# Kernel optimization log

Measured on AMD Instinct MI355X. Metric: run time of the kernel, lower is better.

The kernel has to match this reference:

```python
import jax, jax.numpy as jnp
import numpy as np

N_NODES = 100000
D = 128


def gcn_conv(x, W, b, src, dst, deg_inv_sqrt):
    # PyG GCNConv: linear transform, symmetric-normalized aggregation with self-loops, bias
    h = x @ W  # [N, D_out]
    norm = deg_inv_sqrt[src] * deg_inv_sqrt[dst]  # [E_tot]
    msgs = h[src] * norm[:, None]  # gather + scale  [E_tot, D_out]
    out = jax.ops.segment_sum(msgs, dst, num_segments=x.shape[0])  # scatter-add to targets
    return out + b


def _prep_edges(edge_index, n_nodes):
    # add self-loops (weight 1) and compute deg^{-1/2} over targets (flow source_to_target)
    loops = jnp.arange(n_nodes, dtype=edge_index.dtype)
    src = jnp.concatenate([edge_index[0], loops])
    dst = jnp.concatenate([edge_index[1], loops])
    deg = jax.ops.segment_sum(jnp.ones_like(dst, dtype=jnp.float32), dst, num_segments=n_nodes)
    deg_inv_sqrt = jnp.where(deg > 0, jax.lax.rsqrt(jnp.maximum(deg, 1.0)), 0.0)
    return src, dst, deg_inv_sqrt


def setup_inputs() -> dict:
    key = jax.random.key(0)
    ks = jax.random.split(key, 8)
    node_fts = jax.random.normal(ks[0], (N_NODES, D), dtype=jnp.float32)
    edge_index = jax.random.randint(ks[1], (2, 1600000), 0, N_NODES, dtype=jnp.int64)
    scale = 1.0 / np.sqrt(D)
    W1 = jax.random.uniform(ks[2], (D, D), jnp.float32, -scale, scale)
    b1 = jnp.zeros((D,), jnp.float32)
    W2 = jax.random.uniform(ks[3], (D, D), jnp.float32, -scale, scale)
    b2 = jnp.zeros((D,), jnp.float32)
    W3 = jax.random.uniform(ks[4], (D, D), jnp.float32, -scale, scale)
    b3 = jnp.zeros((D,), jnp.float32)
    return {"node_fts": node_fts, "edge_index": edge_index,
            "W1": W1, "b1": b1, "W2": W2, "b2": b2, "W3": W3, "b3": b3}


def reference(node_fts, edge_index, W1, b1, W2, b2, W3, b3):
    n = node_fts.shape[0]
    src, dst, dinv = _prep_edges(edge_index, n)
    x = jax.nn.relu(gcn_conv(node_fts, W1, b1, src, dst, dinv))
    x = jax.nn.relu(gcn_conv(x, W2, b2, src, dst, dinv))
    x = jax.nn.relu(gcn_conv(x, W3, b3, src, dst, dinv))
    return x
```

## Files before the change

kernel.cpp:

```cpp
#include <hip/hip_runtime.h>

#define NN 100000
#define EE 1600000
#define NPART 8
#define PSZ (NN / NPART)
#define NI4 (EE / 4)
#define SUBW 196
#define NSB (NPART * 64)
#define SCAP 4096
#define RCAP 8192
#define LBCAP 96
#define ROWCAP 64
#define WTB 48

typedef __attribute__((ext_vector_type(8))) short bf16x8;
typedef __attribute__((ext_vector_type(4))) float f32x4;

__device__ inline unsigned int f2bf2(float a, float b) {
    unsigned int ua = __float_as_uint(a);
    unsigned int ub = __float_as_uint(b);
    ua = (ua + 0x7fffu + ((ua >> 16) & 1u)) >> 16;
    ub = (ub + 0x7fffu + ((ub >> 16) & 1u)) >> 16;
    return ua | (ub << 16);
}
__device__ inline unsigned short f2bf(float a) {
    unsigned int u = __float_as_uint(a);
    return (unsigned short)((u + 0x7fffu + ((u >> 16) & 1u)) >> 16);
}
__device__ inline float2 bf2f2(unsigned int u) {
    return make_float2(__uint_as_float(u << 16), __uint_as_float(u & 0xffff0000u));
}


__global__ __launch_bounds__(256) void fbwt_kernel(const int4* __restrict__ src4,
                                                   const int4* __restrict__ dst4,
                                                   int* __restrict__ gcur2,
                                                   uint2* __restrict__ buckets2,
                                                   const float* __restrict__ W1,
                                                   const float* __restrict__ W2,
                                                   const float* __restrict__ W3,
                                                   unsigned short* __restrict__ wt1,
                                                   unsigned short* __restrict__ wt2,
                                                   unsigned short* __restrict__ wt3,
                                                   unsigned int* __restrict__ hb,
                                                   float* __restrict__ dinv) {
    __shared__ uint2 bins[64][LBCAP];
    __shared__ int bcnt[64];
    __shared__ int gbase[64];
    __shared__ float tile[32][33];
    const int bx = blockIdx.x;

    if (bx < WTB) {
        const int m = bx >> 4;
        const int tl = bx & 15;
        const int ti = tl >> 2, tj = tl & 3;
        const float* W = m == 0 ? W1 : (m == 1 ? W2 : W3);
        unsigned short* wt = m == 0 ? wt1 : (m == 1 ? wt2 : wt3);
        const int r = threadIdx.x >> 5, c = threadIdx.x & 31;
#pragma unroll
        for (int rr = r; rr < 32; rr += 8)
            tile[rr][c] = W[(ti * 32 + rr) * 128 + tj * 32 + c];
        __syncthreads();
#pragma unroll
        for (int rr = r; rr < 32; rr += 8)
            wt[(size_t)(tj * 32 + rr) * 128 + ti * 32 + c] = f2bf(tile[c][rr]);
        if (bx == 0) {
            if (threadIdx.x < 64) hb[(size_t)NN * 64 + threadIdx.x] = 0;
            if (threadIdx.x == 64) dinv[NN] = 0.0f;
        }
        return;
    }

    const int fb = bx - WTB;
    const int p = fb >> 6;
    const int c = fb & 63;
    if (threadIdx.x < 64) bcnt[threadIdx.x] = 0;
    __syncthreads();
    const int lo = p * PSZ, hi = lo + PSZ;
    const int chunk4 = NI4 / 64;
    const int a0 = c * chunk4, a1 = a0 + chunk4;
    for (int i = a0 + threadIdx.x; i < a1; i += 256) {
        int4 d4 = dst4[i];
        bool m0 = (d4.x >= lo && d4.x < hi);
        bool m1 = (d4.y >= lo && d4.y < hi);
        bool m2 = (d4.z >= lo && d4.z < hi);
        bool m3 = (d4.w >= lo && d4.w < hi);
        if (!(m0 | m1 | m2 | m3)) continue;
        int4 s4 = src4[i];
        int ss[4] = {s4.x, s4.y, s4.z, s4.w};
        int dd[4] = {d4.x, d4.y, d4.z, d4.w};
        bool mm[4] = {m0, m1, m2, m3};
#pragma unroll
        for (int k = 0; k < 4; ++k) {
            if (!mm[k]) continue;
            int li = (dd[k] - lo) / SUBW;
            int pos = atomicAdd(&bcnt[li], 1);
            if (pos < LBCAP) {
                bins[li][pos] = make_uint2((unsigned)ss[k], (unsigned)dd[k]);
            } else {
                int sb = p * 64 + li;
                int gp = atomicAdd(&gcur2[sb], 1);
                buckets2[(size_t)sb * SCAP + gp] = make_uint2((unsigned)ss[k], (unsigned)dd[k]);
            }
        }
    }
    __syncthreads();
    if (threadIdx.x < 64) {
        int cc = min(bcnt[threadIdx.x], LBCAP);
        gbase[threadIdx.x] = atomicAdd(&gcur2[p * 64 + threadIdx.x], cc);
        bcnt[threadIdx.x] = cc;
    }
    __syncthreads();
    for (int b = 0; b < 64; ++b) {
        const int cc = bcnt[b];
        uint2* outp = buckets2 + (size_t)(p * 64 + b) * SCAP + gbase[b];
        for (int i = threadIdx.x; i < cc; i += 256) outp[i] = bins[b][i];
    }
}


template <bool F32IN, bool SCALE>
__device__ __forceinline__ void gemm_body(int wave, const void* __restrict__ xin,
                                          const unsigned short* __restrict__ wt,
                                          const float* __restrict__ dinv,
                                          unsigned int* __restrict__ hb) {
    const int base = wave * 64;
    if (base >= NN) return;
    const int lane = threadIdx.x & 63;
    const int r = lane & 15;
    const int q = lane >> 4;
    const unsigned short* wrow = wt + (size_t)r * 128 + q * 8;
    bf16x8 wfr[4][8];
#pragma unroll
    for (int kc = 0; kc < 4; ++kc)
#pragma unroll
        for (int nt = 0; nt < 8; ++nt)
            wfr[kc][nt] = *(const bf16x8*)(wrow + (size_t)nt * 16 * 128 + kc * 32);
#pragma unroll
    for (int tt = 0; tt < 4; ++tt) {
        const int m0 = base + tt * 16;
        if (m0 >= NN) break;
        f32x4 acc[8] = {};
#pragma unroll
        for (int kc = 0; kc < 4; ++kc) {
            bf16x8 xf;
            if (F32IN) {
                const float* xrow = (const float*)xin + (size_t)(m0 + r) * 128 + q * 8 + kc * 32;
                float4 a = *(const float4*)xrow;
                float4 b = *(const float4*)(xrow + 4);
                unsigned short tmp[8] = {f2bf(a.x), f2bf(a.y), f2bf(a.z), f2bf(a.w),
                                         f2bf(b.x), f2bf(b.y), f2bf(b.z), f2bf(b.w)};
                xf = *(const bf16x8*)tmp;
            } else {
                const unsigned short* xrow =
                    (const unsigned short*)xin + (size_t)(m0 + r) * 128 + q * 8 + kc * 32;
                xf = *(const bf16x8*)xrow;
            }
#pragma unroll
            for (int nt = 0; nt < 8; ++nt)
                acc[nt] = __builtin_amdgcn_mfma_f32_16x16x32_bf16(wfr[kc][nt], xf, acc[nt], 0, 0, 0);
        }
        const int orow = m0 + r;
        const float dvr = SCALE ? dinv[orow] : 1.0f;
        unsigned int* hrow = hb + (size_t)orow * 64;
#pragma unroll
        for (int nt = 0; nt < 8; ++nt) {
            int n = nt * 16 + q * 4;
            if (SCALE) {
                *(uint2*)(hrow + (n >> 1)) =
                    make_uint2(f2bf2(acc[nt][0] * dvr, acc[nt][1] * dvr),
                               f2bf2(acc[nt][2] * dvr, acc[nt][3] * dvr));
            } else {
                *(uint2*)(hrow + (n >> 1)) =
                    make_uint2(f2bf2(acc[nt][0], acc[nt][1]), f2bf2(acc[nt][2], acc[nt][3]));
            }
        }
    }
}


__global__ __launch_bounds__(256, 2) void sort3_gemm1_kernel(const uint2* __restrict__ buckets2,
                                                             const int* __restrict__ gcur2,
                                                             int* __restrict__ csr,
                                                             int* __restrict__ deg,
                                                             float* __restrict__ dinv,
                                                             const float* __restrict__ x0,
                                                             const unsigned short* __restrict__ wt1,
                                                             unsigned int* __restrict__ hb) {
    __shared__ int hist[256];
    __shared__ int pscan[256];
    __shared__ int lcur[256];
    __shared__ int rs[256];
    __shared__ int staged[RCAP];
    if (blockIdx.x >= 512) {
        const int wave = (blockIdx.x - 512) * 4 + (threadIdx.x >> 6);
        gemm_body<true, false>(wave, (const void*)x0, wt1, nullptr, hb);
        return;
    }
    const int sb = blockIdx.x;
    const int li = sb & 63;
    const int base_node = (sb >> 6) * PSZ + li * SUBW;
    const int nnodes = min(SUBW, PSZ - li * SUBW);
    const int scnt = gcur2[sb];
    const uint2* bk = buckets2 + (size_t)sb * SCAP;
    const int t = threadIdx.x;
    hist[t] = 0;
    __syncthreads();
    for (int i = t; i < scnt; i += 256) atomicAdd(&hist[(int)bk[i].y - base_node], 1);
    __syncthreads();
    const int padded = (t < nnodes) ? ((hist[t] + 7) & ~7) : 0;
    pscan[t] = padded;
    __syncthreads();
    for (int off = 1; off < 256; off <<= 1) {
        int v = (t >= off) ? pscan[t - off] : 0;
        __syncthreads();
        pscan[t] += v;
        __syncthreads();
    }
    const int rstart = pscan[t] - padded;
    lcur[t] = rstart;
    rs[t] = rstart;
    __syncthreads();
    const int total = pscan[255];
    for (int i = t; i < total; i += 256) staged[i] = NN;
    __syncthreads();
    for (int i = t; i < scnt; i += 256) {
        uint2 r = bk[i];
        int pos = atomicAdd(&lcur[(int)r.y - base_node], 1);
        staged[pos] = (int)r.x;
    }
    __syncthreads();
    const int4* staged4 = (const int4*)staged;
    int4* csr4 = (int4*)csr;
    const int4 sv = make_int4(NN, NN, NN, NN);
    for (int i = t; i < nnodes * 16; i += 256) {
        const int n = i >> 4, s = i & 15;
        const int pad = (hist[n] + 7) & ~7;
        int4 v = (s * 4 < pad) ? staged4[(rs[n] >> 2) + s] : sv;
        csr4[((size_t)(base_node + n) << 4) + s] = v;
    }
    if (t < nnodes) {
        int dg = hist[t];
        deg[base_node + t] = dg;
        dinv[base_node + t] = rsqrtf(1.0f + (float)dg);
    }
}

__global__ __launch_bounds__(256, 2) void gemm_kernel(const void* __restrict__ xin,
                                                      const unsigned short* __restrict__ wt,
                                                      const float* __restrict__ dinv,
                                                      unsigned int* __restrict__ hb) {
    const int wave = blockIdx.x * 4 + (threadIdx.x >> 6);
    gemm_body<false, true>(wave, xin, wt, dinv, hb);
}


template <bool BF16OUT, bool WEIGHTED>
__global__ __launch_bounds__(256) void aggregate_kernel(const unsigned int* __restrict__ hb,
                                                        const int* __restrict__ csr,
                                                        const int* __restrict__ deg,
                                                        const float* __restrict__ dinv,
                                                        const float2* __restrict__ bias2,
                                                        void* __restrict__ outp) {
    const int d = blockIdx.x * 4 + (threadIdx.x >> 6);
    const int j = threadIdx.x & 63;
    const int dg = deg[d];
    const float dv = dinv[d];
    int e = d << 6;
    const int end = e + ((dg + 7) & ~7);
    float2 acc;
    {
        float2 s = bf2f2(hb[(size_t)d * 64 + j]);
        if (WEIGHTED) { acc.x = dv * s.x; acc.y = dv * s.y; }
        else          { acc.x = s.x;      acc.y = s.y; }
    }
    for (; e + 16 <= end; e += 16) {
        int4 c0 = *(const int4*)(csr + e);
        int4 c1 = *(const int4*)(csr + e + 4);
        int4 c2 = *(const int4*)(csr + e + 8);
        int4 c3 = *(const int4*)(csr + e + 12);
        unsigned int v0 = hb[(size_t)c0.x * 64 + j];
        unsigned int v1 = hb[(size_t)c0.y * 64 + j];
        unsigned int v2 = hb[(size_t)c0.z * 64 + j];
        unsigned int v3 = hb[(size_t)c0.w * 64 + j];
        unsigned int v4 = hb[(size_t)c1.x * 64 + j];
        unsigned int v5 = hb[(size_t)c1.y * 64 + j];
        unsigned int v6 = hb[(size_t)c1.z * 64 + j];
        unsigned int v7 = hb[(size_t)c1.w * 64 + j];
        unsigned int v8 = hb[(size_t)c2.x * 64 + j];
        unsigned int v9 = hb[(size_t)c2.y * 64 + j];
        unsigned int va = hb[(size_t)c2.z * 64 + j];
        unsigned int vb = hb[(size_t)c2.w * 64 + j];
        unsigned int vc = hb[(size_t)c3.x * 64 + j];
        unsigned int vd = hb[(size_t)c3.y * 64 + j];
        unsigned int ve = hb[(size_t)c3.z * 64 + j];
        unsigned int vf = hb[(size_t)c3.w * 64 + j];
        float2 f0 = bf2f2(v0), f1 = bf2f2(v1), f2 = bf2f2(v2), f3 = bf2f2(v3);
        float2 f4 = bf2f2(v4), f5 = bf2f2(v5), f6 = bf2f2(v6), f7 = bf2f2(v7);
        float2 f8 = bf2f2(v8), f9 = bf2f2(v9), fa = bf2f2(va), fb = bf2f2(vb);
        float2 fc = bf2f2(vc), fd = bf2f2(vd), fe = bf2f2(ve), ff = bf2f2(vf);
        if (WEIGHTED) {
            float w0 = dinv[c0.x], w1 = dinv[c0.y], w2 = dinv[c0.z], w3 = dinv[c0.w];
            float w4 = dinv[c1.x], w5 = dinv[c1.y], w6 = dinv[c1.z], w7 = dinv[c1.w];
            float w8 = dinv[c2.x], w9 = dinv[c2.y], wa = dinv[c2.z], wb = dinv[c2.w];
            float wc = dinv[c3.x], wd = dinv[c3.y], we = dinv[c3.z], wf = dinv[c3.w];
            acc.x += ((w0 * f0.x + w1 * f1.x) + (w2 * f2.x + w3 * f3.x)) +
                     ((w4 * f4.x + w5 * f5.x) + (w6 * f6.x + w7 * f7.x)) +
                     ((w8 * f8.x + w9 * f9.x) + (wa * fa.x + wb * fb.x)) +
                     ((wc * fc.x + wd * fd.x) + (we * fe.x + wf * ff.x));
            acc.y += ((w0 * f0.y + w1 * f1.y) + (w2 * f2.y + w3 * f3.y)) +
                     ((w4 * f4.y + w5 * f5.y) + (w6 * f6.y + w7 * f7.y)) +
                     ((w8 * f8.y + w9 * f9.y) + (wa * fa.y + wb * fb.y)) +
                     ((wc * fc.y + wd * fd.y) + (we * fe.y + wf * ff.y));
        } else {
            acc.x += ((f0.x + f1.x) + (f2.x + f3.x)) + ((f4.x + f5.x) + (f6.x + f7.x)) +
                     ((f8.x + f9.x) + (fa.x + fb.x)) + ((fc.x + fd.x) + (fe.x + ff.x));
            acc.y += ((f0.y + f1.y) + (f2.y + f3.y)) + ((f4.y + f5.y) + (f6.y + f7.y)) +
                     ((f8.y + f9.y) + (fa.y + fb.y)) + ((fc.y + fd.y) + (fe.y + ff.y));
        }
    }
    if (e < end) {
        int4 c0 = *(const int4*)(csr + e);
        int4 c1 = *(const int4*)(csr + e + 4);
        unsigned int v0 = hb[(size_t)c0.x * 64 + j];
        unsigned int v1 = hb[(size_t)c0.y * 64 + j];
        unsigned int v2 = hb[(size_t)c0.z * 64 + j];
        unsigned int v3 = hb[(size_t)c0.w * 64 + j];
        unsigned int v4 = hb[(size_t)c1.x * 64 + j];
        unsigned int v5 = hb[(size_t)c1.y * 64 + j];
        unsigned int v6 = hb[(size_t)c1.z * 64 + j];
        unsigned int v7 = hb[(size_t)c1.w * 64 + j];
        float2 f0 = bf2f2(v0), f1 = bf2f2(v1), f2 = bf2f2(v2), f3 = bf2f2(v3);
        float2 f4 = bf2f2(v4), f5 = bf2f2(v5), f6 = bf2f2(v6), f7 = bf2f2(v7);
        if (WEIGHTED) {
            float w0 = dinv[c0.x], w1 = dinv[c0.y], w2 = dinv[c0.z], w3 = dinv[c0.w];
            float w4 = dinv[c1.x], w5 = dinv[c1.y], w6 = dinv[c1.z], w7 = dinv[c1.w];
            acc.x += ((w0 * f0.x + w1 * f1.x) + (w2 * f2.x + w3 * f3.x)) +
                     ((w4 * f4.x + w5 * f5.x) + (w6 * f6.x + w7 * f7.x));
            acc.y += ((w0 * f0.y + w1 * f1.y) + (w2 * f2.y + w3 * f3.y)) +
                     ((w4 * f4.y + w5 * f5.y) + (w6 * f6.y + w7 * f7.y));
        } else {
            acc.x += ((f0.x + f1.x) + (f2.x + f3.x)) + ((f4.x + f5.x) + (f6.x + f7.x));
            acc.y += ((f0.y + f1.y) + (f2.y + f3.y)) + ((f4.y + f5.y) + (f6.y + f7.y));
        }
    }
    float2 bb = bias2[j];
    float ox = fmaxf(dv * acc.x + bb.x, 0.0f);
    float oy = fmaxf(dv * acc.y + bb.y, 0.0f);
    if (BF16OUT) {
        ((unsigned int*)outp)[(size_t)d * 64 + j] = f2bf2(ox, oy);
    } else {
        ((float2*)outp)[(size_t)d * 64 + j] = make_float2(ox, oy);
    }
}


extern "C" void kernel_launch(void* const* d_in, const int* in_sizes, int n_in,
                              void* d_out, int out_size, void* d_ws, size_t ws_size,
                              hipStream_t stream) {
    const float* x0 = (const float*)d_in[0];
    const int* ei = (const int*)d_in[1];
    const float* W1 = (const float*)d_in[2];
    const float* b1 = (const float*)d_in[3];
    const float* W2 = (const float*)d_in[4];
    const float* b2 = (const float*)d_in[5];
    const float* W3 = (const float*)d_in[6];
    const float* b3 = (const float*)d_in[7];
    float* out = (float*)d_out;

    char* ws = (char*)d_ws;
    size_t off = 0;
    auto alloc = [&](size_t bytes) -> void* {
        off = (off + 511) & ~(size_t)511;
        void* p = ws + off;
        off += bytes;
        return p;
    };
    unsigned int* hb = (unsigned int*)alloc(((size_t)NN + 1) * 64 * 4);
    int* csr = (int*)alloc((size_t)NN * ROWCAP * sizeof(int));
    uint2* buckets2 = (uint2*)alloc((size_t)NSB * SCAP * sizeof(uint2));
    int* deg = (int*)alloc((size_t)NN * sizeof(int));
    float* dinv = (float*)alloc(((size_t)NN + 1) * sizeof(float));
    int* gcur2 = (int*)alloc(NSB * sizeof(int));
    unsigned short* wt1 = (unsigned short*)alloc(128 * 128 * 2);
    unsigned short* wt2 = (unsigned short*)alloc(128 * 128 * 2);
    unsigned short* wt3 = (unsigned short*)alloc(128 * 128 * 2);

    unsigned int* xact = (unsigned int*)d_out;

    const int4* src4 = (const int4*)ei;
    const int4* dst4 = (const int4*)(ei + EE);

    hipMemsetAsync(gcur2, 0, NSB * sizeof(int), stream);
    fbwt_kernel<<<WTB + 512, 256, 0, stream>>>(src4, dst4, gcur2, buckets2,
                                               W1, W2, W3, wt1, wt2, wt3, hb, dinv);
    sort3_gemm1_kernel<<<903, 256, 0, stream>>>(buckets2, gcur2, csr, deg, dinv,
                                                x0, wt1, hb);
    aggregate_kernel<true, true><<<NN / 4, 256, 0, stream>>>(hb, csr, deg, dinv,
                                                             (const float2*)b1, (void*)xact);
    gemm_kernel<<<391, 256, 0, stream>>>((const void*)xact, wt2, dinv, hb);
    aggregate_kernel<true, false><<<NN / 4, 256, 0, stream>>>(hb, csr, deg, dinv,
                                                              (const float2*)b2, (void*)xact);
    gemm_kernel<<<391, 256, 0, stream>>>((const void*)xact, wt3, dinv, hb);
    aggregate_kernel<false, false><<<NN / 4, 256, 0, stream>>>(hb, csr, deg, dinv,
                                                               (const float2*)b3, (void*)out);
}
```

Before: 411.5 us.

## Store compact per-subblock CSR with packed offset/degree info instead of padded rows

Replaces the fixed 64-slot-per-node padded CSR with a compact per-subbucket CSR copied straight from shared memory. Each node gets one packed int holding its row offset and degree. This cuts CSR write and read bandwidth and improves locality of neighbour-index loads. The weighted aggregate becomes a separate kernel, and the packing assumes degree below 256 and offsets that fit in 24 bits.

```diff
diff --git a/kernel.cpp b/kernel.cpp
--- a/kernel.cpp
+++ b/kernel.cpp
@@ -10,7 +10,6 @@
 #define SCAP 4096
 #define RCAP 8192
 #define LBCAP 96
-#define ROWCAP 64
 #define WTB 48
 
 typedef __attribute__((ext_vector_type(8))) short bf16x8;
@@ -182,7 +181,7 @@
 __global__ __launch_bounds__(256, 2) void sort3_gemm1_kernel(const uint2* __restrict__ buckets2,
                                                              const int* __restrict__ gcur2,
                                                              int* __restrict__ csr,
-                                                             int* __restrict__ deg,
+                                                             int* __restrict__ info,
                                                              float* __restrict__ dinv,
                                                              const float* __restrict__ x0,
                                                              const unsigned short* __restrict__ wt1,
@@ -190,7 +189,6 @@
     __shared__ int hist[256];
     __shared__ int pscan[256];
     __shared__ int lcur[256];
-    __shared__ int rs[256];
     __shared__ int staged[RCAP];
     if (blockIdx.x >= 512) {
         const int wave = (blockIdx.x - 512) * 4 + (threadIdx.x >> 6);
@@ -219,7 +217,6 @@
     }
     const int rstart = pscan[t] - padded;
     lcur[t] = rstart;
-    rs[t] = rstart;
     __syncthreads();
     const int total = pscan[255];
     for (int i = t; i < total; i += 256) staged[i] = NN;
@@ -230,18 +227,11 @@
         staged[pos] = (int)r.x;
     }
     __syncthreads();
-    const int4* staged4 = (const int4*)staged;
-    int4* csr4 = (int4*)csr;
-    const int4 sv = make_int4(NN, NN, NN, NN);
-    for (int i = t; i < nnodes * 16; i += 256) {
-        const int n = i >> 4, s = i & 15;
-        const int pad = (hist[n] + 7) & ~7;
-        int4 v = (s * 4 < pad) ? staged4[(rs[n] >> 2) + s] : sv;
-        csr4[((size_t)(base_node + n) << 4) + s] = v;
-    }
+    int4* co = (int4*)(csr + (size_t)sb * RCAP);
+    for (int i = t; i < (total >> 2); i += 256) co[i] = ((const int4*)staged)[i];
     if (t < nnodes) {
         int dg = hist[t];
-        deg[base_node + t] = dg;
+        info[base_node + t] = ((sb * RCAP + rstart) << 8) | dg;
         dinv[base_node + t] = rsqrtf(1.0f + (float)dg);
     }
 }
@@ -255,25 +245,19 @@
 }
 
 
-template <bool BF16OUT, bool WEIGHTED>
+template <bool BF16OUT>
 __global__ __launch_bounds__(256) void aggregate_kernel(const unsigned int* __restrict__ hb,
                                                         const int* __restrict__ csr,
-                                                        const int* __restrict__ deg,
+                                                        const int* __restrict__ info,
                                                         const float* __restrict__ dinv,
                                                         const float2* __restrict__ bias2,
                                                         void* __restrict__ outp) {
     const int d = blockIdx.x * 4 + (threadIdx.x >> 6);
     const int j = threadIdx.x & 63;
-    const int dg = deg[d];
-    const float dv = dinv[d];
-    int e = d << 6;
-    const int end = e + ((dg + 7) & ~7);
-    float2 acc;
-    {
-        float2 s = bf2f2(hb[(size_t)d * 64 + j]);
-        if (WEIGHTED) { acc.x = dv * s.x; acc.y = dv * s.y; }
-        else          { acc.x = s.x;      acc.y = s.y; }
-    }
+    const int ifo = info[d];
+    int e = ifo >> 8;
+    const int end = e + (((ifo & 255) + 7) & ~7);
+    float2 acc = bf2f2(hb[(size_t)d * 64 + j]);
     for (; e + 16 <= end; e += 16) {
         int4 c0 = *(const int4*)(csr + e);
         int4 c1 = *(const int4*)(csr + e + 4);
@@ -299,25 +283,10 @@
         float2 f4 = bf2f2(v4), f5 = bf2f2(v5), f6 = bf2f2(v6), f7 = bf2f2(v7);
         float2 f8 = bf2f2(v8), f9 = bf2f2(v9), fa = bf2f2(va), fb = bf2f2(vb);
         float2 fc = bf2f2(vc), fd = bf2f2(vd), fe = bf2f2(ve), ff = bf2f2(vf);
-        if (WEIGHTED) {
-            float w0 = dinv[c0.x], w1 = dinv[c0.y], w2 = dinv[c0.z], w3 = dinv[c0.w];
-            float w4 = dinv[c1.x], w5 = dinv[c1.y], w6 = dinv[c1.z], w7 = dinv[c1.w];
-            float w8 = dinv[c2.x], w9 = dinv[c2.y], wa = dinv[c2.z], wb = dinv[c2.w];
-            float wc = dinv[c3.x], wd = dinv[c3.y], we = dinv[c3.z], wf = dinv[c3.w];
-            acc.x += ((w0 * f0.x + w1 * f1.x) + (w2 * f2.x + w3 * f3.x)) +
-                     ((w4 * f4.x + w5 * f5.x) + (w6 * f6.x + w7 * f7.x)) +
-                     ((w8 * f8.x + w9 * f9.x) + (wa * fa.x + wb * fb.x)) +
-                     ((wc * fc.x + wd * fd.x) + (we * fe.x + wf * ff.x));
-            acc.y += ((w0 * f0.y + w1 * f1.y) + (w2 * f2.y + w3 * f3.y)) +
-                     ((w4 * f4.y + w5 * f5.y) + (w6 * f6.y + w7 * f7.y)) +
-                     ((w8 * f8.y + w9 * f9.y) + (wa * fa.y + wb * fb.y)) +
-                     ((wc * fc.y + wd * fd.y) + (we * fe.y + wf * ff.y));
-        } else {
-            acc.x += ((f0.x + f1.x) + (f2.x + f3.x)) + ((f4.x + f5.x) + (f6.x + f7.x)) +
-                     ((f8.x + f9.x) + (fa.x + fb.x)) + ((fc.x + fd.x) + (fe.x + ff.x));
-            acc.y += ((f0.y + f1.y) + (f2.y + f3.y)) + ((f4.y + f5.y) + (f6.y + f7.y)) +
-                     ((f8.y + f9.y) + (fa.y + fb.y)) + ((fc.y + fd.y) + (fe.y + ff.y));
-        }
+        acc.x += ((f0.x + f1.x) + (f2.x + f3.x)) + ((f4.x + f5.x) + (f6.x + f7.x)) +
+                 ((f8.x + f9.x) + (fa.x + fb.x)) + ((fc.x + fd.x) + (fe.x + ff.x));
+        acc.y += ((f0.y + f1.y) + (f2.y + f3.y)) + ((f4.y + f5.y) + (f6.y + f7.y)) +
+                 ((f8.y + f9.y) + (fa.y + fb.y)) + ((fc.y + fd.y) + (fe.y + ff.y));
     }
     if (e < end) {
         int4 c0 = *(const int4*)(csr + e);
@@ -332,18 +301,10 @@
         unsigned int v7 = hb[(size_t)c1.w * 64 + j];
         float2 f0 = bf2f2(v0), f1 = bf2f2(v1), f2 = bf2f2(v2), f3 = bf2f2(v3);
         float2 f4 = bf2f2(v4), f5 = bf2f2(v5), f6 = bf2f2(v6), f7 = bf2f2(v7);
-        if (WEIGHTED) {
-            float w0 = dinv[c0.x], w1 = dinv[c0.y], w2 = dinv[c0.z], w3 = dinv[c0.w];
-            float w4 = dinv[c1.x], w5 = dinv[c1.y], w6 = dinv[c1.z], w7 = dinv[c1.w];
-            acc.x += ((w0 * f0.x + w1 * f1.x) + (w2 * f2.x + w3 * f3.x)) +
-                     ((w4 * f4.x + w5 * f5.x) + (w6 * f6.x + w7 * f7.x));
-            acc.y += ((w0 * f0.y + w1 * f1.y) + (w2 * f2.y + w3 * f3.y)) +
-                     ((w4 * f4.y + w5 * f5.y) + (w6 * f6.y + w7 * f7.y));
-        } else {
-            acc.x += ((f0.x + f1.x) + (f2.x + f3.x)) + ((f4.x + f5.x) + (f6.x + f7.x));
-            acc.y += ((f0.y + f1.y) + (f2.y + f3.y)) + ((f4.y + f5.y) + (f6.y + f7.y));
-        }
-    }
+        acc.x += ((f0.x + f1.x) + (f2.x + f3.x)) + ((f4.x + f5.x) + (f6.x + f7.x));
+        acc.y += ((f0.y + f1.y) + (f2.y + f3.y)) + ((f4.y + f5.y) + (f6.y + f7.y));
+    }
+    const float dv = dinv[d];
     float2 bb = bias2[j];
     float ox = fmaxf(dv * acc.x + bb.x, 0.0f);
     float oy = fmaxf(dv * acc.y + bb.y, 0.0f);
@@ -352,6 +313,89 @@
     } else {
         ((float2*)outp)[(size_t)d * 64 + j] = make_float2(ox, oy);
     }
+}
+
+
+__global__ __launch_bounds__(256) void aggregate_w_kernel(const unsigned int* __restrict__ hb,
+                                                          const int* __restrict__ csr,
+                                                          const int* __restrict__ info,
+                                                          const float* __restrict__ dinv,
+                                                          const float2* __restrict__ bias2,
+                                                          unsigned int* __restrict__ outp) {
+    const int d = blockIdx.x * 4 + (threadIdx.x >> 6);
+    const int j = threadIdx.x & 63;
+    const int ifo = info[d];
+    int e = ifo >> 8;
+    const int end = e + (((ifo & 255) + 7) & ~7);
+    const float dv = dinv[d];
+    float2 acc;
+    {
+        float2 s = bf2f2(hb[(size_t)d * 64 + j]);
+        acc.x = dv * s.x;
+        acc.y = dv * s.y;
+    }
+    for (; e + 16 <= end; e += 16) {
+        int4 c0 = *(const int4*)(csr + e);
+        int4 c1 = *(const int4*)(csr + e + 4);
+        int4 c2 = *(const int4*)(csr + e + 8);
+        int4 c3 = *(const int4*)(csr + e + 12);
+        unsigned int v0 = hb[(size_t)c0.x * 64 + j];
+        unsigned int v1 = hb[(size_t)c0.y * 64 + j];
+        unsigned int v2 = hb[(size_t)c0.z * 64 + j];
+        unsigned int v3 = hb[(size_t)c0.w * 64 + j];
+        unsigned int v4 = hb[(size_t)c1.x * 64 + j];
+        unsigned int v5 = hb[(size_t)c1.y * 64 + j];
+        unsigned int v6 = hb[(size_t)c1.z * 64 + j];
+        unsigned int v7 = hb[(size_t)c1.w * 64 + j];
+        unsigned int v8 = hb[(size_t)c2.x * 64 + j];
+        unsigned int v9 = hb[(size_t)c2.y * 64 + j];
+        unsigned int va = hb[(size_t)c2.z * 64 + j];
+        unsigned int vb = hb[(size_t)c2.w * 64 + j];
+        unsigned int vc = hb[(size_t)c3.x * 64 + j];
+        unsigned int vd = hb[(size_t)c3.y * 64 + j];
+        unsigned int ve = hb[(size_t)c3.z * 64 + j];
+        unsigned int vf = hb[(size_t)c3.w * 64 + j];
+        float w0 = dinv[c0.x], w1 = dinv[c0.y], w2 = dinv[c0.z], w3 = dinv[c0.w];
+        float w4 = dinv[c1.x], w5 = dinv[c1.y], w6 = dinv[c1.z], w7 = dinv[c1.w];
+        float w8 = dinv[c2.x], w9 = dinv[c2.y], wa = dinv[c2.z], wb = dinv[c2.w];
+        float wc = dinv[c3.x], wd = dinv[c3.y], we = dinv[c3.z], wf = dinv[c3.w];
+        float2 f0 = bf2f2(v0), f1 = bf2f2(v1), f2 = bf2f2(v2), f3 = bf2f2(v3);
+        float2 f4 = bf2f2(v4), f5 = bf2f2(v5), f6 = bf2f2(v6), f7 = bf2f2(v7);
+        float2 f8 = bf2f2(v8), f9 = bf2f2(v9), fa = bf2f2(va), fb = bf2f2(vb);
+        float2 fc = bf2f2(vc), fd = bf2f2(vd), fe = bf2f2(ve), ff = bf2f2(vf);
+        acc.x += ((w0 * f0.x + w1 * f1.x) + (w2 * f2.x + w3 * f3.x)) +
+                 ((w4 * f4.x + w5 * f5.x) + (w6 * f6.x + w7 * f7.x)) +
+                 ((w8 * f8.x + w9 * f9.x) + (wa * fa.x + wb * fb.x)) +
+                 ((wc * fc.x + wd * fd.x) + (we * fe.x + wf * ff.x));
+        acc.y += ((w0 * f0.y + w1 * f1.y) + (w2 * f2.y + w3 * f3.y)) +
+                 ((w4 * f4.y + w5 * f5.y) + (w6 * f6.y + w7 * f7.y)) +
+                 ((w8 * f8.y + w9 * f9.y) + (wa * fa.y + wb * fb.y)) +
+                 ((wc * fc.y + wd * fd.y) + (we * fe.y + wf * ff.y));
+    }
+    if (e < end) {
+        int4 c0 = *(const int4*)(csr + e);
+        int4 c1 = *(const int4*)(csr + e + 4);
+        unsigned int v0 = hb[(size_t)c0.x * 64 + j];
+        unsigned int v1 = hb[(size_t)c0.y * 64 + j];
+        unsigned int v2 = hb[(size_t)c0.z * 64 + j];
+        unsigned int v3 = hb[(size_t)c0.w * 64 + j];
+        unsigned int v4 = hb[(size_t)c1.x * 64 + j];
+        unsigned int v5 = hb[(size_t)c1.y * 64 + j];
+        unsigned int v6 = hb[(size_t)c1.z * 64 + j];
+        unsigned int v7 = hb[(size_t)c1.w * 64 + j];
+        float w0 = dinv[c0.x], w1 = dinv[c0.y], w2 = dinv[c0.z], w3 = dinv[c0.w];
+        float w4 = dinv[c1.x], w5 = dinv[c1.y], w6 = dinv[c1.z], w7 = dinv[c1.w];
+        float2 f0 = bf2f2(v0), f1 = bf2f2(v1), f2 = bf2f2(v2), f3 = bf2f2(v3);
+        float2 f4 = bf2f2(v4), f5 = bf2f2(v5), f6 = bf2f2(v6), f7 = bf2f2(v7);
+        acc.x += ((w0 * f0.x + w1 * f1.x) + (w2 * f2.x + w3 * f3.x)) +
+                 ((w4 * f4.x + w5 * f5.x) + (w6 * f6.x + w7 * f7.x));
+        acc.y += ((w0 * f0.y + w1 * f1.y) + (w2 * f2.y + w3 * f3.y)) +
+                 ((w4 * f4.y + w5 * f5.y) + (w6 * f6.y + w7 * f7.y));
+    }
+    float2 bb = bias2[j];
+    float ox = fmaxf(dv * acc.x + bb.x, 0.0f);
+    float oy = fmaxf(dv * acc.y + bb.y, 0.0f);
+    outp[(size_t)d * 64 + j] = f2bf2(ox, oy);
 }
 
 
@@ -377,9 +421,9 @@
         return p;
     };
     unsigned int* hb = (unsigned int*)alloc(((size_t)NN + 1) * 64 * 4);
-    int* csr = (int*)alloc((size_t)NN * ROWCAP * sizeof(int));
+    int* csr = (int*)alloc((size_t)NSB * RCAP * sizeof(int));
     uint2* buckets2 = (uint2*)alloc((size_t)NSB * SCAP * sizeof(uint2));
-    int* deg = (int*)alloc((size_t)NN * sizeof(int));
+    int* info = (int*)alloc((size_t)NN * sizeof(int));
     float* dinv = (float*)alloc(((size_t)NN + 1) * sizeof(float));
     int* gcur2 = (int*)alloc(NSB * sizeof(int));
     unsigned short* wt1 = (unsigned short*)alloc(128 * 128 * 2);
@@ -394,14 +438,14 @@
     hipMemsetAsync(gcur2, 0, NSB * sizeof(int), stream);
     fbwt_kernel<<<WTB + 512, 256, 0, stream>>>(src4, dst4, gcur2, buckets2,
                                                W1, W2, W3, wt1, wt2, wt3, hb, dinv);
-    sort3_gemm1_kernel<<<903, 256, 0, stream>>>(buckets2, gcur2, csr, deg, dinv,
+    sort3_gemm1_kernel<<<903, 256, 0, stream>>>(buckets2, gcur2, csr, info, dinv,
                                                 x0, wt1, hb);
-    aggregate_kernel<true, true><<<NN / 4, 256, 0, stream>>>(hb, csr, deg, dinv,
-                                                             (const float2*)b1, (void*)xact);
+    aggregate_w_kernel<<<NN / 4, 256, 0, stream>>>(hb, csr, info, dinv,
+                                                   (const float2*)b1, xact);
     gemm_kernel<<<391, 256, 0, stream>>>((const void*)xact, wt2, dinv, hb);
-    aggregate_kernel<true, false><<<NN / 4, 256, 0, stream>>>(hb, csr, deg, dinv,
-                                                              (const float2*)b2, (void*)xact);
+    aggregate_kernel<true><<<NN / 4, 256, 0, stream>>>(hb, csr, info, dinv,
+                                                       (const float2*)b2, (void*)xact);
     gemm_kernel<<<391, 256, 0, stream>>>((const void*)xact, wt3, dinv, hb);
-    aggregate_kernel<false, false><<<NN / 4, 256, 0, stream>>>(hb, csr, deg, dinv,
-                                                               (const float2*)b3, (void*)out);
-}
+    aggregate_kernel<false><<<NN / 4, 256, 0, stream>>>(hb, csr, info, dinv,
+                                                        (const float2*)b3, (void*)out);
+}
```

Measured after the change: 399.2 us, median of 2. 1.03x faster.
